# Kernel optimization log

Measured on AMD Instinct MI355X. Metric: run time of the kernel, lower is better.

Reference implementation:

```python
import jax, jax.numpy as jnp
import numpy as np

B, Q, G = 32, 4000, 100
C1, C2, C3 = 4, 32, 8
ALPHA, GAMMA = 0.25, 2.0
OTA_K = 5
CENTER_RADIUS = 2.5
COST_BBOX = 1.0
COST_GIOU = 1.0
COST_CLASS = 1.0 / 3.0  # forward sets self.cost_class = 1/len(heads) = 1/3


def box_xyxy_to_cxcywh(b):
    x0, y0, x1, y1 = b[..., 0], b[..., 1], b[..., 2], b[..., 3]
    return jnp.stack([(x0 + x1) * 0.5, (y0 + y1) * 0.5, x1 - x0, y1 - y0], axis=-1)


def box_cxcywh_to_xyxy(b):
    cx, cy, w, h = b[..., 0], b[..., 1], b[..., 2], b[..., 3]
    return jnp.stack([cx - 0.5 * w, cy - 0.5 * h, cx + 0.5 * w, cy + 0.5 * h], axis=-1)


def box_iou(a, b):
    # a [Q,4], b [G,4] in xyxy -> iou, union [Q,G]
    area_a = (a[:, 2] - a[:, 0]) * (a[:, 3] - a[:, 1])
    area_b = (b[:, 2] - b[:, 0]) * (b[:, 3] - b[:, 1])
    lt = jnp.maximum(a[:, None, :2], b[None, :, :2])
    rb = jnp.minimum(a[:, None, 2:], b[None, :, 2:])
    wh = jnp.clip(rb - lt, 0.0)
    inter = wh[..., 0] * wh[..., 1]
    union = area_a[:, None] + area_b[None, :] - inter
    return inter / union, union


def generalized_box_iou(a, b):
    iou, union = box_iou(a, b)
    lt = jnp.minimum(a[:, None, :2], b[None, :, :2])
    rb = jnp.maximum(a[:, None, 2:], b[None, :, 2:])
    wh = jnp.clip(rb - lt, 0.0)
    area = wh[..., 0] * wh[..., 1]
    return iou - (area - union) / area


def get_in_boxes_info(boxes_c, gts_c):
    # boxes_c [Q,4] cxcywh anchors, gts_c [G,4] cxcywh gts
    xy = box_cxcywh_to_xyxy(gts_c)  # [G,4]
    ax, ay = boxes_c[:, 0:1], boxes_c[:, 1:2]  # [Q,1]
    in_box = (ax > xy[:, 0]) & (ax < xy[:, 2]) & (ay > xy[:, 1]) & (ay < xy[:, 3])  # [Q,G]
    w = xy[:, 2] - xy[:, 0]
    h = xy[:, 3] - xy[:, 1]
    cx, cy = gts_c[:, 0], gts_c[:, 1]
    in_ctr = ((ax > cx - CENTER_RADIUS * w) & (ax < cx + CENTER_RADIUS * w) &
              (ay > cy - CENTER_RADIUS * h) & (ay < cy + CENTER_RADIUS * h))
    fg_mask = jnp.any(in_box, axis=1) | jnp.any(in_ctr, axis=1)  # [Q]
    return fg_mask, in_box & in_ctr


def compute_cost(l1, l2, l3, pb, gb, isz, t1, t2, t3):
    fg_mask, in_bc = get_in_boxes_info(box_xyxy_to_cxcywh(pb), box_xyxy_to_cxcywh(gb))
    ious, _ = box_iou(pb, gb)

    def focal_cost(logits, labels):
        p = jax.nn.sigmoid(logits)
        neg = (1.0 - ALPHA) * p ** GAMMA * (-jnp.log(1.0 - p + 1e-8))
        pos = ALPHA * (1.0 - p) ** GAMMA * (-jnp.log(p + 1e-8))
        return (pos - neg)[:, labels]  # [Q,G]

    cc = focal_cost(l1, t1) + focal_cost(l2, t2) + focal_cost(l3, t3)
    nb = pb / isz[None, :]
    ng = gb / isz[None, :]
    cost_bbox = jnp.sum(jnp.abs(nb[:, None, :] - ng[None, :, :]), axis=-1)  # L1 cdist [Q,G]
    cost_giou = -generalized_box_iou(pb, gb)
    cost = (COST_BBOX * cost_bbox + COST_CLASS * cc + COST_GIOU * cost_giou
            + 100.0 * (~in_bc).astype(cost_bbox.dtype))
    cost = cost + 10000.0 * (~fg_mask)[:, None].astype(cost.dtype)
    return cost, ious


def dynamic_k_matching(cost, ious):
    q, g = cost.shape
    topk_ious, _ = jax.lax.top_k(ious.T, OTA_K)  # [G,k]
    dynamic_ks = jnp.clip(topk_ious.sum(1).astype(jnp.int32), 1, None)  # [G]
    # top dynamic_ks[g] lowest-cost queries per gt (dynamic_ks <= OTA_K since ious in [0,1])
    _, pos_idx = jax.lax.top_k(-cost.T, OTA_K)  # [G,k]
    valid = (jnp.arange(OTA_K)[None, :] < dynamic_ks[:, None]).astype(cost.dtype)
    m = jnp.zeros_like(cost).at[pos_idx, jnp.arange(g)[:, None]].add(valid)

    def resolve(m_, c_):
        # anchors matched to >1 gt keep only their min-cost gt
        multi = m_.sum(1) > 1
        one = jax.nn.one_hot(jnp.argmin(c_, axis=1), g, dtype=m_.dtype)
        return jnp.where(multi[:, None], one, m_)

    m = resolve(m, cost)

    def cond(st):
        return jnp.any(st[0].sum(0) == 0)

    def body(st):
        m_, c_ = st
        c_ = c_ + jnp.where((m_.sum(1) > 0)[:, None], 1e5, 0.0)  # penalize already-matched queries
        unmatched = m_.sum(0) == 0  # [G]
        one = jax.nn.one_hot(jnp.argmin(c_, axis=0), q, dtype=m_.dtype, axis=0)  # [Q,G]
        m_ = jnp.where(unmatched[None, :], one, m_)
        m_ = resolve(m_, c_)
        return (m_, c_)

    m, c = jax.lax.while_loop(cond, body, (m, cost))
    selected = m.sum(1) > 0            # [Q] bool: which queries are matched
    gt_idx = jnp.argmax(m, axis=1)     # [Q] gt index per query (valid where selected)
    matched_qidx = jnp.argmin(jnp.where(m > 0, c, jnp.inf), axis=0)  # [G]
    return m, selected, gt_idx, matched_qidx


def reference(pred_logits_1, pred_logits_2, pred_logits_3, pred_boxes, gt_boxes_xyxy, img_size, labels_1, labels_2, labels_3):
    def per_image(l1, l2, l3, pb, gb, isz, t1, t2, t3):
        cost, ious = compute_cost(l1, l2, l3, pb, gb, isz, t1, t2, t3)
        m, selected, gt_idx, matched_qidx = dynamic_k_matching(cost, ious)
        return m, selected, gt_idx, matched_qidx, cost
    return jax.vmap(per_image)(pred_logits_1, pred_logits_2, pred_logits_3,
                               pred_boxes, gt_boxes_xyxy, img_size,
                               labels_1, labels_2, labels_3)


def setup_inputs() -> dict:
    key = jax.random.key(0)
    ks = jax.random.split(key, 8)

    def rand_boxes(k, n):
        k1, k2 = jax.random.split(k)
        cxcy = jax.random.uniform(k1, (B, n, 2), minval=32.0, maxval=480.0)
        wh = jax.random.uniform(k2, (B, n, 2), minval=16.0, maxval=128.0)
        return jnp.concatenate([cxcy - wh * 0.5, cxcy + wh * 0.5], axis=-1)

    return {
        "pred_logits_1": jax.random.normal(ks[0], (B, Q, C1), jnp.float32),
        "pred_logits_2": jax.random.normal(ks[1], (B, Q, C2), jnp.float32),
        "pred_logits_3": jax.random.normal(ks[2], (B, Q, C3), jnp.float32),
        "pred_boxes": rand_boxes(ks[3], Q),
        "gt_boxes_xyxy": rand_boxes(ks[4], G),
        "img_size": jnp.full((B, 4), 512.0, jnp.float32),
        "labels_1": jax.random.randint(ks[5], (B, G), 0, C1),
        "labels_2": jax.random.randint(ks[6], (B, G), 0, C2),
        "labels_3": jax.random.randint(ks[7], (B, G), 0, C3),
    }
```

## Files before the change

### kernel.cpp

```cpp
#include <hip/hip_runtime.h>
#include <math.h>
#include <stdint.h>

#define NB 32
#define NQ 4000
#define NG 100
#define NC1 4
#define NC2 32
#define NC3 8
#define NCT 44
#define GCH 25
#define SLK 16
#define MTH 512

static const size_t OFF_M    = 0;
static const size_t OFF_SEL  = (size_t)NB * NQ * NG;
static const size_t OFF_GTI  = OFF_SEL + (size_t)NB * NQ;
static const size_t OFF_MQ   = OFF_GTI + (size_t)NB * NQ;
static const size_t OFF_COST = OFF_MQ + (size_t)NB * NG;

__device__ __forceinline__ float focal_diff(float x) {
    float p   = 1.0f / (1.0f + expf(-x));
    float neg = 0.75f * (p * p) * (-logf(1.0f - p + 1e-8f));
    float pos = 0.25f * ((1.0f - p) * (1.0f - p)) * (-logf(p + 1e-8f));
    return pos - neg;
}

__device__ __forceinline__ unsigned ordered_bits(float f) {
    unsigned u = __float_as_uint(f);
    return (u & 0x80000000u) ? ~u : (u | 0x80000000u);
}

__global__ __launch_bounds__(256) void focal_kernel(
    const float* __restrict__ l1, const float* __restrict__ l2, const float* __restrict__ l3,
    float* __restrict__ FDT)
{
    const int b  = blockIdx.y;
    const int q0 = blockIdx.x * 64;
    const int tid = threadIdx.x;
    __shared__ float tile[64][NCT + 1];

    for (int idx = tid; idx < 64 * NC1; idx += 256) {
        const int qi = idx >> 2, c = idx & 3;
        const int q = q0 + qi;
        if (q < NQ) tile[qi][c] = focal_diff(l1[((size_t)b * NQ + q) * NC1 + c]);
    }
    for (int idx = tid; idx < 64 * NC2; idx += 256) {
        const int qi = idx >> 5, c = idx & 31;
        const int q = q0 + qi;
        if (q < NQ) tile[qi][NC1 + c] = focal_diff(l2[((size_t)b * NQ + q) * NC2 + c]);
    }
    for (int idx = tid; idx < 64 * NC3; idx += 256) {
        const int qi = idx >> 3, c = idx & 7;
        const int q = q0 + qi;
        if (q < NQ) tile[qi][NC1 + NC2 + c] = focal_diff(l3[((size_t)b * NQ + q) * NC3 + c]);
    }
    __syncthreads();

    for (int idx = tid; idx < NCT * 64; idx += 256) {
        const int c = idx >> 6, qi = idx & 63;
        const int q = q0 + qi;
        if (q < NQ) FDT[((size_t)b * NCT + c) * NQ + q] = tile[qi][c];
    }
}

__global__ __launch_bounds__(256) void mask_kernel(
    const float* __restrict__ pb, const float* __restrict__ gbx,
    uint4* __restrict__ bmout, float* __restrict__ fgout)
{
    const int b   = blockIdx.y;
    const int tid = threadIdx.x;

    __shared__ float s_ib[NG][4];
    __shared__ float s_ic[NG][4];

    if (tid < NG) {
        const int g = tid;
        const float x0 = gbx[((size_t)b * NG + g) * 4 + 0];
        const float y0 = gbx[((size_t)b * NG + g) * 4 + 1];
        const float x1 = gbx[((size_t)b * NG + g) * 4 + 2];
        const float y1 = gbx[((size_t)b * NG + g) * 4 + 3];
        const float cx = (x0 + x1) * 0.5f, cy = (y0 + y1) * 0.5f;
        const float w0 = x1 - x0, h0 = y1 - y0;
        const float bx0 = cx - 0.5f * w0, bx1 = cx + 0.5f * w0;
        const float by0 = cy - 0.5f * h0, by1 = cy + 0.5f * h0;
        s_ib[g][0] = bx0; s_ib[g][1] = by0; s_ib[g][2] = bx1; s_ib[g][3] = by1;
        const float w = bx1 - bx0, h = by1 - by0;
        s_ic[g][0] = cx - 2.5f * w; s_ic[g][1] = cx + 2.5f * w;
        s_ic[g][2] = cy - 2.5f * h; s_ic[g][3] = cy + 2.5f * h;
    }
    __syncthreads();

    const int q = blockIdx.x * 256 + tid;
    if (q >= NQ) return;

    const float4 pv = reinterpret_cast<const float4*>(pb)[(size_t)b * NQ + q];
    const float ax = (pv.x + pv.z) * 0.5f, ay = (pv.y + pv.w) * 0.5f;

    unsigned bm[4] = {0u, 0u, 0u, 0u};
    bool fg = false;
    for (int g = 0; g < NG; ++g) {
        const bool ib = (ax > s_ib[g][0]) && (ax < s_ib[g][2]) && (ay > s_ib[g][1]) && (ay < s_ib[g][3]);
        const bool ic = (ax > s_ic[g][0]) && (ax < s_ic[g][1]) && (ay > s_ic[g][2]) && (ay < s_ic[g][3]);
        fg = fg || ib || ic;
        if (ib && ic) bm[g >> 5] |= (1u << (g & 31));
    }
    bmout[(size_t)b * NQ + q] = make_uint4(bm[0], bm[1], bm[2], bm[3]);
    fgout[(size_t)b * NQ + q] = fg ? 0.0f : 10000.0f;
}

__global__ __launch_bounds__(256) void cost_kernel(
    const float* __restrict__ pb, const float* __restrict__ gbx, const float* __restrict__ img,
    const int* __restrict__ t1, const int* __restrict__ t2, const int* __restrict__ t3,
    const float* __restrict__ FDT, const uint4* __restrict__ bmin, const float* __restrict__ fgin,
    float* __restrict__ costT)
{
    const int b   = blockIdx.y;
    const int g0  = blockIdx.z * GCH;
    const int tid = threadIdx.x;

    __shared__ float s_ng[GCH][4];
    __shared__ float s_gx[GCH][4];
    __shared__ float s_ab[GCH];
    __shared__ int   s_lab[GCH][3];
    __shared__ float s_isz[4];

    if (tid < 4) s_isz[tid] = img[b * 4 + tid];
    if (tid < GCH) {
        const int g = g0 + tid;
        const float x0 = gbx[((size_t)b * NG + g) * 4 + 0];
        const float y0 = gbx[((size_t)b * NG + g) * 4 + 1];
        const float x1 = gbx[((size_t)b * NG + g) * 4 + 2];
        const float y1 = gbx[((size_t)b * NG + g) * 4 + 3];
        s_gx[tid][0] = x0; s_gx[tid][1] = y0; s_gx[tid][2] = x1; s_gx[tid][3] = y1;
        s_ab[tid] = (x1 - x0) * (y1 - y0);
        s_ng[tid][0] = x0 / img[b * 4 + 0];
        s_ng[tid][1] = y0 / img[b * 4 + 1];
        s_ng[tid][2] = x1 / img[b * 4 + 2];
        s_ng[tid][3] = y1 / img[b * 4 + 3];
        s_lab[tid][0] = t1[b * NG + g];
        s_lab[tid][1] = NC1 + t2[b * NG + g];
        s_lab[tid][2] = NC1 + NC2 + t3[b * NG + g];
    }
    __syncthreads();

    const int q = blockIdx.x * 256 + tid;
    if (q >= NQ) return;

    const float4 pv = reinterpret_cast<const float4*>(pb)[(size_t)b * NQ + q];
    const float p0 = pv.x, p1 = pv.y, p2 = pv.z, p3 = pv.w;
    const float areaA = (p2 - p0) * (p3 - p1);
    const float n0 = p0 / s_isz[0], n1 = p1 / s_isz[1], n2 = p2 / s_isz[2], n3 = p3 / s_isz[3];

    const uint4 bm4 = bmin[(size_t)b * NQ + q];
    const unsigned bm[4] = {bm4.x, bm4.y, bm4.z, bm4.w};
    const float fgadd = fgin[(size_t)b * NQ + q];

    const float* F = FDT + (size_t)b * NCT * NQ + q;
    float* ct = costT + (size_t)b * NG * NQ + q + (size_t)g0 * NQ;
#pragma unroll 5
    for (int gl = 0; gl < GCH; ++gl) {
        const int g = g0 + gl;
        const float f1 = F[(size_t)s_lab[gl][0] * NQ];
        const float f2 = F[(size_t)s_lab[gl][1] * NQ];
        const float f3 = F[(size_t)s_lab[gl][2] * NQ];
        float cb = fabsf(n0 - s_ng[gl][0]);
        cb = cb + fabsf(n1 - s_ng[gl][1]);
        cb = cb + fabsf(n2 - s_ng[gl][2]);
        cb = cb + fabsf(n3 - s_ng[gl][3]);
        const float gx0 = s_gx[gl][0], gy0 = s_gx[gl][1], gx1 = s_gx[gl][2], gy1 = s_gx[gl][3];
        const float ltx = fmaxf(p0, gx0), lty = fmaxf(p1, gy0);
        const float rbx = fminf(p2, gx1), rby = fminf(p3, gy1);
        const float iw = fmaxf(rbx - ltx, 0.0f), ih = fmaxf(rby - lty, 0.0f);
        const float inter = iw * ih;
        const float uni = areaA + s_ab[gl] - inter;
        const float iou = inter / uni;
        const float ex0 = fminf(p0, gx0), ey0 = fminf(p1, gy0);
        const float ex1 = fmaxf(p2, gx1), ey1 = fmaxf(p3, gy1);
        const float ew = fmaxf(ex1 - ex0, 0.0f), eh = fmaxf(ey1 - ey0, 0.0f);
        const float ea = ew * eh;
        const float giou = iou - (ea - uni) / ea;
        const float cc = (f1 + f2) + f3;
        const bool inbc = (bm[g >> 5] >> (g & 31)) & 1u;
        float cost = cb;
        cost = cost + 0.33333334f * cc;
        cost = cost + (-giou);
        cost = cost + (inbc ? 0.0f : 100.0f);
        cost = cost + fgadd;
        ct[(size_t)gl * NQ] = cost;
    }
}

template <bool MAXSEL>
__device__ __forceinline__ bool better(float av, int ai, float bv, int bi) {
    if (MAXSEL) return (av > bv) || (av == bv && ai < bi);
    else        return (av < bv) || (av == bv && ai < bi);
}

template <bool MAXSEL>
__device__ __forceinline__ void ins5(float (&v)[5], int (&id)[5], float nv, int ni) {
    if (!better<MAXSEL>(nv, ni, v[4], id[4])) return;
    v[4] = nv; id[4] = ni;
#pragma unroll
    for (int j = 4; j > 0; --j) {
        if (better<MAXSEL>(v[j], id[j], v[j - 1], id[j - 1])) {
            float tv = v[j]; v[j] = v[j - 1]; v[j - 1] = tv;
            int   ti = id[j]; id[j] = id[j - 1]; id[j - 1] = ti;
        }
    }
}

template <bool MAXSEL>
__device__ __forceinline__ void merge5(float (&v)[5], int (&id)[5], float (&ov)[5], int (&oi)[5]) {
#pragma unroll
    for (int r = 0; r < 5; ++r) {
        float bv = v[0]; int bi = id[0];
#pragma unroll
        for (int off = 32; off >= 1; off >>= 1) {
            float xv = __shfl_xor(bv, off, 64);
            int   xi = __shfl_xor(bi, off, 64);
            if (better<MAXSEL>(xv, xi, bv, bi)) { bv = xv; bi = xi; }
        }
        ov[r] = bv; oi[r] = bi;
        if (id[0] == bi) {
            v[0] = v[1]; id[0] = id[1];
            v[1] = v[2]; id[1] = id[2];
            v[2] = v[3]; id[2] = id[3];
            v[3] = v[4]; id[3] = id[4];
            v[4] = MAXSEL ? -INFINITY : INFINITY; id[4] = 0x7fffffff;
        }
    }
}

__device__ __forceinline__ void push_max5i(float (&v)[5], int (&id)[5], float t, int it) {
#pragma unroll
    for (int i = 0; i < 5; ++i) {
        const bool b = t > v[i];
        const float nv = b ? t : v[i];
        const float nt = b ? v[i] : t;
        const int ni  = b ? it : id[i];
        const int nit = b ? id[i] : it;
        v[i] = nv; id[i] = ni; t = nt; it = nit;
    }
}

#define CHUNK 1000

#define CE(i, j) { const unsigned long long _a = kk[i], _b = kk[j]; \
                   const bool _s = _b < _a; \
                   kk[i] = _s ? _b : _a; kk[j] = _s ? _a : _b; }

__global__ __launch_bounds__(256, 2) void col_topk_kernel(
    const float* __restrict__ pb, const float* __restrict__ gbx, const float* __restrict__ costT,
    int* __restrict__ grc, int* __restrict__ grnew, int* __restrict__ grsl)
{
    const int g = blockIdx.x, b = blockIdx.y;
    const int tid = threadIdx.x, lane = tid & 63, wave = tid >> 6;

    __shared__ float              s_v[4][5];
    __shared__ int                s_i[4][5];
    __shared__ unsigned long long s_ck[4][SLK];

    const float gx0 = gbx[((size_t)b * NG + g) * 4 + 0];
    const float gy0 = gbx[((size_t)b * NG + g) * 4 + 1];
    const float gx1 = gbx[((size_t)b * NG + g) * 4 + 2];
    const float gy1 = gbx[((size_t)b * NG + g) * 4 + 3];
    const float areaB = (gx1 - gx0) * (gy1 - gy0);
    const float4* PB = reinterpret_cast<const float4*>(pb) + (size_t)b * NQ;
    const float* CT = costT + (size_t)b * NG * NQ + (size_t)g * NQ;

    const int q0 = wave * CHUNK;

    {
        unsigned long long kk[16];
#pragma unroll
        for (int i = 0; i < 16; ++i) {
            const bool live = (i < 15) || (lane < 40);
            const int q = q0 + i * 64 + lane;
            const float c = live ? CT[q] : 0.0f;
            kk[i] = live ? ((((unsigned long long)ordered_bits(c)) << 32) | (unsigned)q)
                         : ~0ull;
        }

        CE(0,1)  CE(2,3)  CE(4,5)  CE(6,7)  CE(8,9)  CE(10,11) CE(12,13) CE(14,15)
        CE(0,2)  CE(1,3)  CE(4,6)  CE(5,7)  CE(8,10) CE(9,11)  CE(12,14) CE(13,15)
        CE(1,2)  CE(5,6)  CE(9,10) CE(13,14)
        CE(0,4)  CE(1,5)  CE(2,6)  CE(3,7)  CE(8,12) CE(9,13)  CE(10,14) CE(11,15)
        CE(2,4)  CE(3,5)  CE(10,12) CE(11,13)
        CE(1,2)  CE(3,4)  CE(5,6)  CE(9,10) CE(11,12) CE(13,14)
        CE(0,8)  CE(1,9)  CE(2,10) CE(3,11) CE(4,12)  CE(5,13)  CE(6,14)  CE(7,15)
        CE(4,8)  CE(5,9)  CE(6,10) CE(7,11)
        CE(2,4)  CE(3,5)  CE(6,8)  CE(7,9)  CE(10,12) CE(11,13)
        CE(1,2)  CE(3,4)  CE(5,6)  CE(7,8)  CE(9,10)  CE(11,12) CE(13,14)

        for (int r = 0; r < SLK; ++r) {
            unsigned long long bk = kk[0];
#pragma unroll
            for (int off = 32; off >= 1; off >>= 1) {
                const unsigned long long xk = __shfl_xor(bk, off, 64);
                if (xk < bk) bk = xk;
            }
            if (lane == 0) s_ck[wave][r] = bk;
            if (kk[0] == bk) {
#pragma unroll
                for (int j = 0; j < 15; ++j) kk[j] = kk[j + 1];
                kk[15] = ~0ull;
            }
        }
    }

    {
        const int q1 = q0 + CHUNK;
        float tv[5]; int ti[5];
#pragma unroll
        for (int k = 0; k < 5; ++k) { tv[k] = -INFINITY; ti[k] = 0x7fffffff; }
        for (int base = q0; base < q1; base += 64) {
            const int q = base + lane;
            if (q < q1) {
                const float4 p = PB[q];
                const float ltx = fmaxf(p.x, gx0), lty = fmaxf(p.y, gy0);
                const float rbx = fminf(p.z, gx1), rby = fminf(p.w, gy1);
                const float iw = fmaxf(rbx - ltx, 0.0f), ih = fmaxf(rby - lty, 0.0f);
                const float inter = iw * ih;
                const float areaA = (p.z - p.x) * (p.w - p.y);
                const float uni = areaA + areaB - inter;
                push_max5i(tv, ti, inter / uni, q);
            }
        }
        float ov[5]; int oi[5];
        merge5<true>(tv, ti, ov, oi);
        if (lane == 0) {
#pragma unroll
            for (int k = 0; k < 5; ++k) { s_v[wave][k] = ov[k]; s_i[wave][k] = oi[k]; }
        }
    }
    __syncthreads();

    if (tid == 0) {
        float tv[5]; int ti[5];
#pragma unroll
        for (int k = 0; k < 5; ++k) { tv[k] = -INFINITY; ti[k] = 0x7fffffff; }
        for (int w = 0; w < 4; ++w)
#pragma unroll
            for (int k = 0; k < 5; ++k) ins5<true>(tv, ti, s_v[w][k], s_i[w][k]);
        const float s = ((((tv[0] + tv[1]) + tv[2]) + tv[3]) + tv[4]);
        int dk = (int)s;
        if (dk < 1) dk = 1;

        int h0 = 0, h1 = 0, h2 = 0, h3 = 0;
        int* SL = grsl + ((size_t)b * NG + g) * SLK;
        for (int k = 0; k < SLK; ++k) {
            unsigned long long bk = ~0ull; int bw = 0;
            if (h0 < SLK && s_ck[0][h0] < bk) { bk = s_ck[0][h0]; bw = 0; }
            if (h1 < SLK && s_ck[1][h1] < bk) { bk = s_ck[1][h1]; bw = 1; }
            if (h2 < SLK && s_ck[2][h2] < bk) { bk = s_ck[2][h2]; bw = 2; }
            if (h3 < SLK && s_ck[3][h3] < bk) { bk = s_ck[3][h3]; bw = 3; }
            if (bw == 0) h0++; else if (bw == 1) h1++; else if (bw == 2) h2++; else h3++;
            const int bi = (int)(unsigned)(bk & 0xffffffffull);
            SL[k] = bi;
            if (k < dk) {
                atomicAdd(&grc[b * NQ + bi], 1);
                grnew[b * NQ + bi] = g;
            }
        }
    }
}

__device__ __forceinline__ float pen_add(float v, int k) {
    while (k-- > 0) v += 100000.0f;
    return v;
}

__global__ __launch_bounds__(MTH) void match_kernel(
    const float* __restrict__ costT, const int* __restrict__ grc, const int* __restrict__ grnew,
    const int* __restrict__ grsl,
    float* __restrict__ out, int* __restrict__ rm_out)
{
    const int b = blockIdx.x, tid = threadIdx.x;
    const int lane = tid & 63, wave = tid >> 6;

    __shared__ short              rmatch[NQ];
    __shared__ short              rnew[NQ];
    __shared__ short              tmat[NQ];
    __shared__ int                rc[NQ];
    __shared__ int                colc[NG];
    __shared__ unsigned long long colkey[NG];
    __shared__ short              sl[NG * SLK];
    __shared__ short              wl[2][1024];
    __shared__ int                wlc[2];
    __shared__ int                flag;

    const float* CT = costT + (size_t)b * NG * NQ;

    if (tid == 0) { wlc[0] = 0; wlc[1] = 0; }
    if (tid < NG) colc[tid] = 0;
    __syncthreads();

    for (int q = tid; q < NQ; q += MTH) {
        rmatch[q] = -1;
        const int r = grc[b * NQ + q];
        rc[q] = r;
        rnew[q] = (short)grnew[b * NQ + q];
        if (r > 0) { const int i = atomicAdd(&wlc[0], 1); wl[0][i] = (short)q; }
    }
    for (int i = tid; i < NG * SLK; i += MTH) sl[i] = (short)grsl[(size_t)b * NG * SLK + i];
    __syncthreads();

    int L = 2000;
    for (int iter = 0; iter < 2000; ++iter) {
        const int p = iter & 1;
        const int n = wlc[p];
        for (int i = tid; i < n; i += MTH) {
            const int q = (int)wl[p][i];
            const int rcq = atomicExch(&rc[q], 0);
            if (rcq == 0) continue;
            const int oldm = rmatch[q];
            const int c = rcq + (oldm >= 0 ? 1 : 0);
            int nm;
            if (c == 1) nm = (int)rnew[q];
            else {
                const int kp = (oldm >= 0) ? (iter - (int)tmat[q]) : 0;
                float bv = INFINITY; nm = 0;
                for (int g = 0; g < NG; ++g) {
                    const float v = pen_add(CT[(size_t)g * NQ + q], kp);
                    if (v < bv) { bv = v; nm = g; }
                }
            }
            rmatch[q] = (short)nm;
            if (oldm < 0) { tmat[q] = (short)iter; atomicAdd(&colc[nm], 1); }
            else if (oldm != nm) { atomicSub(&colc[oldm], 1); atomicAdd(&colc[nm], 1); }
        }
        if (tid == 0) { wlc[p ^ 1] = 0; flag = 0; }
        __syncthreads();

        for (int g = wave; g < NG; g += (MTH / 64)) {
            if (colc[g] != 0) continue;
            if (lane == 0) flag = 1;
            int cand = -1;
            if (lane < SLK) {
                const int qq = (int)sl[g * SLK + lane];
                if (rmatch[qq] < 0) cand = qq;
            }
            const unsigned long long bal = __ballot(cand >= 0);
            int bi;
            if (bal != 0ull) {
                const int src = __ffsll(bal) - 1;
                bi = __shfl(cand, src, 64);
            } else {
                float bv = INFINITY; bi = 0x7fffffff;
                for (int base = 0; base < NQ; base += 64) {
                    const int q = base + lane;
                    if (q < NQ) {
                        const int kp = (rmatch[q] >= 0) ? (iter + 1 - (int)tmat[q]) : 0;
                        const float v = pen_add(CT[(size_t)g * NQ + q], kp);
                        if (v < bv || (v == bv && q < bi)) { bv = v; bi = q; }
                    }
                }
#pragma unroll
                for (int off = 32; off >= 1; off >>= 1) {
                    const float xv = __shfl_xor(bv, off, 64);
                    const int   xi = __shfl_xor(bi, off, 64);
                    if (xv < bv || (xv == bv && xi < bi)) { bv = xv; bi = xi; }
                }
            }
            if (lane == 0) {
                atomicAdd(&rc[bi], 1);
                rnew[bi] = (short)g;
                const int i = atomicAdd(&wlc[p ^ 1], 1);
                wl[p ^ 1][i] = (short)bi;
            }
        }
        __syncthreads();
        if (!flag) { L = iter; break; }
    }

    if (tid < NG) colkey[tid] = ~0ull;
    __syncthreads();
    for (int q = tid; q < NQ; q += MTH) {
        const int m = rmatch[q];
        out[OFF_SEL + (size_t)b * NQ + q] = (m >= 0) ? 1.0f : 0.0f;
        out[OFF_GTI + (size_t)b * NQ + q] = (float)(m >= 0 ? m : 0);
        rm_out[b * NQ + q] = m;
        if (m >= 0) {
            const float v = pen_add(CT[(size_t)m * NQ + q], L - (int)tmat[q]);
            const unsigned long long key = ((unsigned long long)ordered_bits(v) << 32) | (unsigned)q;
            atomicMin(&colkey[m], key);
        }
    }
    __syncthreads();
    if (tid < NG) out[OFF_MQ + (size_t)b * NG + tid] = (float)(unsigned)(colkey[tid] & 0xffffffffull);
}

__global__ __launch_bounds__(256) void write_out_kernel(
    const float* __restrict__ costT, const int* __restrict__ rm, float* __restrict__ out)
{
    const int b  = blockIdx.y;
    const int q0 = blockIdx.x * 64;
    __shared__ float tile[NG][65];
    __shared__ short srm[64];
    const float* CT = costT + (size_t)b * NG * NQ;
    for (int idx = threadIdx.x; idx < NG * 64; idx += 256) {
        const int g = idx >> 6, qi = idx & 63;
        const int q = q0 + qi;
        if (q < NQ) tile[g][qi] = CT[(size_t)g * NQ + q];
    }
    if (threadIdx.x < 64) {
        const int q = q0 + threadIdx.x;
        srm[threadIdx.x] = (q < NQ) ? (short)rm[b * NQ + q] : (short)-1;
    }
    __syncthreads();
    float* OC = out + OFF_COST + (size_t)b * NQ * NG;
    float* OM = out + OFF_M    + (size_t)b * NQ * NG;
    for (int idx = threadIdx.x; idx < 64 * NG; idx += 256) {
        const int qi = idx / NG, g = idx - qi * NG;
        const int q = q0 + qi;
        if (q < NQ) {
            OC[(size_t)q * NG + g] = tile[g][qi];
            OM[(size_t)q * NG + g] = (srm[qi] == g) ? 1.0f : 0.0f;
        }
    }
}

extern "C" void kernel_launch(void* const* d_in, const int* in_sizes, int n_in,
                              void* d_out, int out_size, void* d_ws, size_t ws_size,
                              hipStream_t stream)
{
    const float* l1  = (const float*)d_in[0];
    const float* l2  = (const float*)d_in[1];
    const float* l3  = (const float*)d_in[2];
    const float* pb  = (const float*)d_in[3];
    const float* gbx = (const float*)d_in[4];
    const float* img = (const float*)d_in[5];
    const int*   t1  = (const int*)d_in[6];
    const int*   t2  = (const int*)d_in[7];
    const int*   t3  = (const int*)d_in[8];
    float* out = (float*)d_out;

    char* ws = (char*)d_ws;
    float* costT = (float*)ws;                                   ws += (size_t)NB * NG * NQ * sizeof(float);
    int*   rm    = (int*)ws;                                     ws += (size_t)NB * NQ * sizeof(int);
    int*   grc   = (int*)ws;                                     ws += (size_t)NB * NQ * sizeof(int);
    int*   grnew = (int*)ws;                                     ws += (size_t)NB * NQ * sizeof(int);
    uint4* bmws  = (uint4*)ws;                                   ws += (size_t)NB * NQ * sizeof(uint4);
    float* fgws  = (float*)ws;                                   ws += (size_t)NB * NQ * sizeof(float);
    int*   grsl  = (int*)ws;

    float* FDT = out + OFF_COST;

    hipMemsetAsync(grc, 0, (size_t)NB * NQ * sizeof(int), stream);

    dim3 fg((NQ + 63) / 64, NB);
    focal_kernel<<<fg, 256, 0, stream>>>(l1, l2, l3, FDT);

    dim3 mk((NQ + 255) / 256, NB);
    mask_kernel<<<mk, 256, 0, stream>>>(pb, gbx, bmws, fgws);

    dim3 cg((NQ + 255) / 256, NB, 4);
    cost_kernel<<<cg, 256, 0, stream>>>(pb, gbx, img, t1, t2, t3, FDT, bmws, fgws, costT);

    dim3 kg(NG, NB);
    col_topk_kernel<<<kg, 256, 0, stream>>>(pb, gbx, costT, grc, grnew, grsl);

    match_kernel<<<NB, MTH, 0, stream>>>(costT, grc, grnew, grsl, out, rm);

    dim3 wg((NQ + 63) / 64, NB);
    write_out_kernel<<<wg, 256, 0, stream>>>(costT, rm, out);
}
```

Before: 317.8 us.

## Write row-major cost output directly from cost kernel, shrink final pass to mask

The cost kernel now writes each cost value to both the transposed workspace and the row-major output slot, which removes the final shared-memory transpose that reread the whole cost matrix. The last kernel only expands the matched index into the one-hot mask using float4 stores. The focal scratch moves to the mask region of the output because the cost region is now written early. Each thread's direct output writes hit 25 consecutive floats per row with a 400-byte stride across lanes, so they coalesce poorly.

```diff
diff --git a/kernel.cpp b/kernel.cpp
--- a/kernel.cpp
+++ b/kernel.cpp
@@ -113,7 +113,7 @@
     const float* __restrict__ pb, const float* __restrict__ gbx, const float* __restrict__ img,
     const int* __restrict__ t1, const int* __restrict__ t2, const int* __restrict__ t3,
     const float* __restrict__ FDT, const uint4* __restrict__ bmin, const float* __restrict__ fgin,
-    float* __restrict__ costT)
+    float* __restrict__ costT, float* __restrict__ outc)
 {
     const int b   = blockIdx.y;
     const int g0  = blockIdx.z * GCH;
@@ -158,6 +158,7 @@
 
     const float* F = FDT + (size_t)b * NCT * NQ + q;
     float* ct = costT + (size_t)b * NG * NQ + q + (size_t)g0 * NQ;
+    float* oc = outc + ((size_t)b * NQ + q) * NG + g0;
 #pragma unroll 5
     for (int gl = 0; gl < GCH; ++gl) {
         const int g = g0 + gl;
@@ -188,6 +189,7 @@
         cost = cost + (inbc ? 0.0f : 100.0f);
         cost = cost + fgadd;
         ct[(size_t)gl * NQ] = cost;
+        oc[gl] = cost;
     }
 }
 
@@ -491,33 +493,23 @@
     if (tid < NG) out[OFF_MQ + (size_t)b * NG + tid] = (float)(unsigned)(colkey[tid] & 0xffffffffull);
 }
 
-__global__ __launch_bounds__(256) void write_out_kernel(
-    const float* __restrict__ costT, const int* __restrict__ rm, float* __restrict__ out)
-{
-    const int b  = blockIdx.y;
-    const int q0 = blockIdx.x * 64;
-    __shared__ float tile[NG][65];
-    __shared__ short srm[64];
-    const float* CT = costT + (size_t)b * NG * NQ;
-    for (int idx = threadIdx.x; idx < NG * 64; idx += 256) {
-        const int g = idx >> 6, qi = idx & 63;
-        const int q = q0 + qi;
-        if (q < NQ) tile[g][qi] = CT[(size_t)g * NQ + q];
-    }
-    if (threadIdx.x < 64) {
-        const int q = q0 + threadIdx.x;
-        srm[threadIdx.x] = (q < NQ) ? (short)rm[b * NQ + q] : (short)-1;
-    }
-    __syncthreads();
-    float* OC = out + OFF_COST + (size_t)b * NQ * NG;
-    float* OM = out + OFF_M    + (size_t)b * NQ * NG;
-    for (int idx = threadIdx.x; idx < 64 * NG; idx += 256) {
-        const int qi = idx / NG, g = idx - qi * NG;
-        const int q = q0 + qi;
-        if (q < NQ) {
-            OC[(size_t)q * NG + g] = tile[g][qi];
-            OM[(size_t)q * NG + g] = (srm[qi] == g) ? 1.0f : 0.0f;
-        }
+__global__ __launch_bounds__(256) void m_expand_kernel(
+    const int* __restrict__ rm, float* __restrict__ out)
+{
+    const int b = blockIdx.y;
+    const int q = blockIdx.x * 256 + threadIdx.x;
+    if (q >= NQ) return;
+    const int m = rm[b * NQ + q];
+    float4* OM = reinterpret_cast<float4*>(out + OFF_M + ((size_t)b * NQ + q) * NG);
+#pragma unroll
+    for (int j = 0; j < NG / 4; ++j) {
+        const int g0 = j * 4;
+        float4 v;
+        v.x = (m == g0 + 0) ? 1.0f : 0.0f;
+        v.y = (m == g0 + 1) ? 1.0f : 0.0f;
+        v.z = (m == g0 + 2) ? 1.0f : 0.0f;
+        v.w = (m == g0 + 3) ? 1.0f : 0.0f;
+        OM[j] = v;
     }
 }
 
@@ -545,7 +537,8 @@
     float* fgws  = (float*)ws;                                   ws += (size_t)NB * NQ * sizeof(float);
     int*   grsl  = (int*)ws;
 
-    float* FDT = out + OFF_COST;
+    float* FDT = out + OFF_M;
+    float* OC  = out + OFF_COST;
 
     hipMemsetAsync(grc, 0, (size_t)NB * NQ * sizeof(int), stream);
 
@@ -556,13 +549,13 @@
     mask_kernel<<<mk, 256, 0, stream>>>(pb, gbx, bmws, fgws);
 
     dim3 cg((NQ + 255) / 256, NB, 4);
-    cost_kernel<<<cg, 256, 0, stream>>>(pb, gbx, img, t1, t2, t3, FDT, bmws, fgws, costT);
+    cost_kernel<<<cg, 256, 0, stream>>>(pb, gbx, img, t1, t2, t3, FDT, bmws, fgws, costT, OC);
 
     dim3 kg(NG, NB);
     col_topk_kernel<<<kg, 256, 0, stream>>>(pb, gbx, costT, grc, grnew, grsl);
 
     match_kernel<<<NB, MTH, 0, stream>>>(costT, grc, grnew, grsl, out, rm);
 
-    dim3 wg((NQ + 63) / 64, NB);
-    write_out_kernel<<<wg, 256, 0, stream>>>(costT, rm, out);
-}
+    dim3 wg((NQ + 255) / 256, NB);
+    m_expand_kernel<<<wg, 256, 0, stream>>>(rm, out);
+}
```

New measurement: 371.4 us. +16.9%, slower.
